# Kernel optimization log

Measured on AMD Instinct MI355X. Metric: run time of the kernel, lower is better.

The kernel has to match this reference:

```python
import jax, jax.numpy as jnp
import numpy as np

B, M, N = 8, 1024, 2048          # batch, check nodes, variable nodes
NUM_ITERS = 5
ROW_DEGREE = 8                   # ones per check row (sparse Tanner graph)
NEG_BIG = -1e30 - 1.0


def _make_H():
    rng = np.random.RandomState(0)
    H = np.zeros((M, N), dtype=np.int32)
    for i in range(M):
        cols = rng.choice(N, size=ROW_DEGREE, replace=False)
        H[i, cols] = 1
    # guarantee every variable node has at least one check
    empty = np.where(H.sum(0) == 0)[0]
    for j in empty:
        H[rng.randint(M), j] = 1
    return H


def setup_inputs() -> dict:
    key = jax.random.key(0)
    k1, _ = jax.random.split(key)
    soft_input = jax.random.normal(k1, (B, N), dtype=jnp.float32) * 2.0
    check_weight = jnp.full((1,), -1.07, dtype=jnp.float32)  # NMS normalized factor
    H = jnp.asarray(_make_H())
    return {"soft_input": soft_input, "check_weight": check_weight, "H": H}


def reference(soft_input, check_weight, H):
    Hf = H.astype(jnp.float32)                      # [M, N]
    back = jnp.where(Hf == 0, NEG_BIG, 0.0)[None]   # [1, M, N]
    supp = (1.0 - Hf)[None]                         # [1, M, N]
    alpha = jax.nn.softplus(check_weight)           # NMS scalar normalization

    def body(cv, _):
        # --- variable-to-check: vc = (sum_m cv + llr) on edges, minus own message
        col_sum = jnp.sum(cv, axis=1) + soft_input            # [B, N]
        vc = col_sum[:, None, :] * Hf - cv                    # [B, M, N]
        # --- check-to-variable: min-sum with min/submin trick
        vc_abs = jnp.clip(jnp.abs(vc), 0.0, 1e30)
        dec = -vc_abs + back                                  # mask off non-edges
        top2 = jax.lax.top_k(dec, 2)[0]                       # [B, M, 2]
        mn = (-top2[..., 0])[:, :, None] * Hf                 # row min, broadcast on edges
        sub = (-top2[..., 1])[:, :, None] * Hf                # row second min
        result = jnp.where(vc_abs > mn, mn, sub)              # exclude-self min
        sign = jnp.sign(supp + vc)                            # non-edges -> sign(+1)
        row_prod = jnp.prod(sign, axis=2)[:, :, None] * Hf
        result_sign = row_prod * sign                         # product of other signs
        cv_new = result * jax.lax.stop_gradient(result_sign) * alpha
        return cv_new, None

    cv0 = jnp.zeros((soft_input.shape[0], Hf.shape[0], Hf.shape[1]), jnp.float32)
    cv_final, _ = jax.lax.scan(body, cv0, None, length=NUM_ITERS)
    soft_output = soft_input + jnp.sum(cv_final, axis=1)      # [B, N] posterior LLRs
    return soft_output
```

## Files before the change

### kernel.cpp

```cpp
#include <hip/hip_runtime.h>
#include <hip/hip_bf16.h>


#define M_CHECK 1024
#define N_VAR   2048
#define BATCH   8
#define MAXD    12
#define NUM_ITERS 5
#define FXS 16384.0f
#define FXI (1.0f / 16384.0f)

__global__ __launch_bounds__(256) void build_rows_kernel(
    const int* __restrict__ H, int* __restrict__ deg,
    int* __restrict__ row_cols_T)
{
    const int m    = blockIdx.x * 4 + (threadIdx.x >> 6);
    const int lane = threadIdx.x & 63;
    const unsigned long long below = (1ULL << lane) - 1ULL;
    const int4* __restrict__ H4 = (const int4*)(H + m * N_VAR);

    int base = 0;
    for (int c = 0; c < N_VAR; c += 256) {
        int4 h = H4[(c >> 2) + lane];
        unsigned long long m0 = __ballot(h.x != 0);
        unsigned long long m1 = __ballot(h.y != 0);
        unsigned long long m2 = __ballot(h.z != 0);
        unsigned long long m3 = __ballot(h.w != 0);
        int pb = __popcll(m0 & below) + __popcll(m1 & below)
               + __popcll(m2 & below) + __popcll(m3 & below);
        int b0 = (int)((m0 >> lane) & 1);
        int b1 = (int)((m1 >> lane) & 1);
        int b2 = (int)((m2 >> lane) & 1);
        int col = c + 4 * lane;
        int r = base + pb;
        if (h.x) { if (r < MAXD) row_cols_T[r * M_CHECK + m] = col; }
        r += b0;
        if (h.y) { if (r < MAXD) row_cols_T[r * M_CHECK + m] = col + 1; }
        r += b1;
        if (h.z) { if (r < MAXD) row_cols_T[r * M_CHECK + m] = col + 2; }
        r += b2;
        if (h.w) { if (r < MAXD) row_cols_T[r * M_CHECK + m] = col + 3; }
        base += __popcll(m0) + __popcll(m1) + __popcll(m2) + __popcll(m3);
    }
    if (lane == 0) deg[m] = (base < MAXD) ? base : MAXD;
}

__global__ __launch_bounds__(1024) void decode_kernel(
    const float* __restrict__ soft_input, const float* __restrict__ check_weight,
    const int* __restrict__ deg, const int* __restrict__ row_cols_T,
    float* __restrict__ out)
{
    __shared__ int   acc[3][N_VAR];
    __shared__ float soft_s[N_VAR];

    const int b = blockIdx.x;
    const int t = threadIdx.x;
    const float alpha = log1pf(expf(check_weight[0]));

    const int n0 = t, n1 = t + 1024;
    const float soft0 = soft_input[b * N_VAR + n0];
    const float soft1 = soft_input[b * N_VAR + n1];
    soft_s[n0] = soft0;  soft_s[n1] = soft1;
    acc[0][n0] = 0; acc[0][n1] = 0;
    acc[1][n0] = 0; acc[1][n1] = 0;
    acc[2][n0] = 0; acc[2][n1] = 0;

    const int dm = deg[t];
    int   cols[MAXD];
    float cv[MAXD];
#pragma unroll
    for (int d = 0; d < MAXD; ++d) {
        cols[d] = (d < dm) ? row_cols_T[d * M_CHECK + t] : 0;
        cv[d]   = 0.f;
    }
    __syncthreads();

    float softc[MAXD];
#pragma unroll
    for (int d = 0; d < MAXD; ++d)
        softc[d] = (d < dm) ? soft_s[cols[d]] : 0.f;

#pragma unroll
    for (int it = 0; it < NUM_ITERS; ++it) {
        const int gb = it % 3;
        const int sb = (it + 1) % 3;
        const int rb = (it + 2) % 3;

        float vcs[MAXD];
        float mn1 = 1e38f, mn2 = 1e38f;
        unsigned sx = 0u;
        bool zr = false;
#pragma unroll
        for (int d = 0; d < MAXD; ++d) {
            if (d < dm) {
                float colsum = softc[d] + (float)acc[gb][cols[d]] * FXI;
                float vc = colsum - cv[d];
                vcs[d] = vc;
                float a = fminf(fabsf(vc), 1e30f);
                if (a < mn1) { mn2 = mn1; mn1 = a; }
                else if (a < mn2) { mn2 = a; }
                sx ^= (__float_as_uint(vc) & 0x80000000u);
                zr |= (vc == 0.f);
            }
        }
        const float zmul = zr ? 0.f : alpha;
#pragma unroll
        for (int d = 0; d < MAXD; ++d) {
            if (d < dm) {
                float vc  = vcs[d];
                float a   = fminf(fabsf(vc), 1e30f);
                float res = (a > mn1) ? mn1 : mn2;
                unsigned others = sx ^ (__float_as_uint(vc) & 0x80000000u);
                float v = res * zmul;
                float cvn = __uint_as_float(__float_as_uint(v) ^ others);
                cv[d] = cvn;
                atomicAdd(&acc[sb][cols[d]], __float2int_rn(cvn * FXS));
            }
        }
        acc[rb][n0] = 0;
        acc[rb][n1] = 0;
        __syncthreads();
    }

    const int fb = NUM_ITERS % 3;
    out[b * N_VAR + n0] = soft0 + (float)acc[fb][n0] * FXI;
    out[b * N_VAR + n1] = soft1 + (float)acc[fb][n1] * FXI;
}

extern "C" void kernel_launch(void* const* d_in, const int* in_sizes, int n_in,
                              void* d_out, int out_size, void* d_ws, size_t ws_size,
                              hipStream_t stream)
{
    const float* soft_input   = (const float*)d_in[0];
    const float* check_weight = (const float*)d_in[1];
    const int*   H            = (const int*)d_in[2];
    float*       out          = (float*)d_out;

    int* deg        = (int*)d_ws;
    int* row_cols_T = deg + M_CHECK;

    build_rows_kernel<<<M_CHECK / 4, 256, 0, stream>>>(H, deg, row_cols_T);
    decode_kernel<<<BATCH, 1024, 0, stream>>>(
        soft_input, check_weight, deg, row_cols_T, out);
}
```

Before: 20.87 us.

## Process two batch items per block and peel the first decoding iteration

Each 1024-thread block now decodes two batch elements, reusing the loaded column indices and sharing each barrier across both, with launches cut from 8 blocks to 4. The first iteration is peeled because cv and the accumulators start at zero, so it reads soft inputs directly and skips the shared-memory gathers. This doubles the serial work per block on a grid already far smaller than the CU count, and doubles shared memory and register use, in exchange for fewer syncs per element and more independent work per thread for latency hiding.

```diff
diff --git a/kernel.cpp b/kernel.cpp
--- a/kernel.cpp
+++ b/kernel.cpp
@@ -5,6 +5,7 @@
 #define M_CHECK 1024
 #define N_VAR   2048
 #define BATCH   8
+#define BPB     2
 #define MAXD    12
 #define NUM_ITERS 5
 #define FXS 16384.0f
@@ -50,53 +51,51 @@
     const int* __restrict__ deg, const int* __restrict__ row_cols_T,
     float* __restrict__ out)
 {
-    __shared__ int   acc[3][N_VAR];
-    __shared__ float soft_s[N_VAR];
+    __shared__ int   acc[BPB][3][N_VAR];
+    __shared__ float soft_s[BPB][N_VAR];
 
-    const int b = blockIdx.x;
-    const int t = threadIdx.x;
+    const int b0 = blockIdx.x * BPB;
+    const int t  = threadIdx.x;
     const float alpha = log1pf(expf(check_weight[0]));
 
     const int n0 = t, n1 = t + 1024;
-    const float soft0 = soft_input[b * N_VAR + n0];
-    const float soft1 = soft_input[b * N_VAR + n1];
-    soft_s[n0] = soft0;  soft_s[n1] = soft1;
-    acc[0][n0] = 0; acc[0][n1] = 0;
-    acc[1][n0] = 0; acc[1][n1] = 0;
-    acc[2][n0] = 0; acc[2][n1] = 0;
+    const float s00 = soft_input[ b0      * N_VAR + n0];
+    const float s01 = soft_input[ b0      * N_VAR + n1];
+    const float s10 = soft_input[(b0 + 1) * N_VAR + n0];
+    const float s11 = soft_input[(b0 + 1) * N_VAR + n1];
+    soft_s[0][n0] = s00;  soft_s[0][n1] = s01;
+    soft_s[1][n0] = s10;  soft_s[1][n1] = s11;
+#pragma unroll
+    for (int q = 0; q < 3; ++q) {
+        acc[0][q][n0] = 0; acc[0][q][n1] = 0;
+        acc[1][q][n0] = 0; acc[1][q][n1] = 0;
+    }
 
     const int dm = deg[t];
-    int   cols[MAXD];
-    float cv[MAXD];
+    int cols[MAXD];
+#pragma unroll
+    for (int d = 0; d < MAXD; ++d)
+        cols[d] = (d < dm) ? row_cols_T[d * M_CHECK + t] : 0;
+    __syncthreads();
+
+    float softc[BPB][MAXD];
 #pragma unroll
     for (int d = 0; d < MAXD; ++d) {
-        cols[d] = (d < dm) ? row_cols_T[d * M_CHECK + t] : 0;
-        cv[d]   = 0.f;
+        softc[0][d] = (d < dm) ? soft_s[0][cols[d]] : 0.f;
+        softc[1][d] = (d < dm) ? soft_s[1][cols[d]] : 0.f;
     }
-    __syncthreads();
 
-    float softc[MAXD];
-#pragma unroll
-    for (int d = 0; d < MAXD; ++d)
-        softc[d] = (d < dm) ? soft_s[cols[d]] : 0.f;
+    float cv[BPB][MAXD];
 
 #pragma unroll
-    for (int it = 0; it < NUM_ITERS; ++it) {
-        const int gb = it % 3;
-        const int sb = (it + 1) % 3;
-        const int rb = (it + 2) % 3;
-
-        float vcs[MAXD];
+    for (int p = 0; p < BPB; ++p) {
         float mn1 = 1e38f, mn2 = 1e38f;
-        unsigned sx = 0u;
-        bool zr = false;
+        unsigned sx = 0u;  bool zr = false;
 #pragma unroll
         for (int d = 0; d < MAXD; ++d) {
             if (d < dm) {
-                float colsum = softc[d] + (float)acc[gb][cols[d]] * FXI;
-                float vc = colsum - cv[d];
-                vcs[d] = vc;
-                float a = fminf(fabsf(vc), 1e30f);
+                float vc = softc[p][d];
+                float a  = fminf(fabsf(vc), 1e30f);
                 if (a < mn1) { mn2 = mn1; mn1 = a; }
                 else if (a < mn2) { mn2 = a; }
                 sx ^= (__float_as_uint(vc) & 0x80000000u);
@@ -107,24 +106,67 @@
 #pragma unroll
         for (int d = 0; d < MAXD; ++d) {
             if (d < dm) {
-                float vc  = vcs[d];
+                float vc  = softc[p][d];
                 float a   = fminf(fabsf(vc), 1e30f);
                 float res = (a > mn1) ? mn1 : mn2;
-                unsigned others = sx ^ (__float_as_uint(vc) & 0x80000000u);
-                float v = res * zmul;
-                float cvn = __uint_as_float(__float_as_uint(v) ^ others);
-                cv[d] = cvn;
-                atomicAdd(&acc[sb][cols[d]], __float2int_rn(cvn * FXS));
+                unsigned o = sx ^ (__float_as_uint(vc) & 0x80000000u);
+                float v   = res * zmul;
+                float cvn = __uint_as_float(__float_as_uint(v) ^ o);
+                cv[p][d] = cvn;
+                atomicAdd(&acc[p][1][cols[d]], __float2int_rn(cvn * FXS));
             }
         }
-        acc[rb][n0] = 0;
-        acc[rb][n1] = 0;
+    }
+    __syncthreads();
+
+#pragma unroll
+    for (int it = 1; it < NUM_ITERS; ++it) {
+        const int gb = it % 3, sb = (it + 1) % 3, rb = (it + 2) % 3;
+#pragma unroll
+        for (int p = 0; p < BPB; ++p) {
+            float vcs[MAXD];
+            float mn1 = 1e38f, mn2 = 1e38f;
+            unsigned sx = 0u;  bool zr = false;
+#pragma unroll
+            for (int d = 0; d < MAXD; ++d) {
+                if (d < dm) {
+                    float vc = softc[p][d]
+                             + (float)acc[p][gb][cols[d]] * FXI - cv[p][d];
+                    vcs[d] = vc;
+                    float a = fminf(fabsf(vc), 1e30f);
+                    if (a < mn1) { mn2 = mn1; mn1 = a; }
+                    else if (a < mn2) { mn2 = a; }
+                    sx ^= (__float_as_uint(vc) & 0x80000000u);
+                    zr |= (vc == 0.f);
+                }
+            }
+            const float zmul = zr ? 0.f : alpha;
+#pragma unroll
+            for (int d = 0; d < MAXD; ++d) {
+                if (d < dm) {
+                    float vc  = vcs[d];
+                    float a   = fminf(fabsf(vc), 1e30f);
+                    float res = (a > mn1) ? mn1 : mn2;
+                    unsigned o = sx ^ (__float_as_uint(vc) & 0x80000000u);
+                    float v   = res * zmul;
+                    float cvn = __uint_as_float(__float_as_uint(v) ^ o);
+                    cv[p][d] = cvn;
+                    atomicAdd(&acc[p][sb][cols[d]], __float2int_rn(cvn * FXS));
+                }
+            }
+        }
+        if (it != NUM_ITERS - 1) {
+            acc[0][rb][n0] = 0; acc[0][rb][n1] = 0;
+            acc[1][rb][n0] = 0; acc[1][rb][n1] = 0;
+        }
         __syncthreads();
     }
 
     const int fb = NUM_ITERS % 3;
-    out[b * N_VAR + n0] = soft0 + (float)acc[fb][n0] * FXI;
-    out[b * N_VAR + n1] = soft1 + (float)acc[fb][n1] * FXI;
+    out[ b0      * N_VAR + n0] = s00 + (float)acc[0][fb][n0] * FXI;
+    out[ b0      * N_VAR + n1] = s01 + (float)acc[0][fb][n1] * FXI;
+    out[(b0 + 1) * N_VAR + n0] = s10 + (float)acc[1][fb][n0] * FXI;
+    out[(b0 + 1) * N_VAR + n1] = s11 + (float)acc[1][fb][n1] * FXI;
 }
 
 extern "C" void kernel_launch(void* const* d_in, const int* in_sizes, int n_in,
@@ -140,6 +182,6 @@
     int* row_cols_T = deg + M_CHECK;
 
     build_rows_kernel<<<M_CHECK / 4, 256, 0, stream>>>(H, deg, row_cols_T);
-    decode_kernel<<<BATCH, 1024, 0, stream>>>(
+    decode_kernel<<<BATCH / BPB, 1024, 0, stream>>>(
         soft_input, check_weight, deg, row_cols_T, out);
 }
```

Result: slower. 29.81 us (+42.9%).
